# Performance work log

Measured on AMD Instinct MI355X. Metric: run time of the kernel, lower is better.

Reference implementation:

```python
import jax, jax.numpy as jnp
import numpy as np

P = 64        # patch size
NATOMS = 256  # dictionary atoms
N = 262144    # signal length
K = 262081    # npatches = N - P + 1 (stride-1 sliding patches)
M = 512       # measurement rows of A


def setup_inputs() -> dict:
    key = jax.random.key(0)
    k0, k1, k2, k3, k4, k5, k6 = jax.random.split(key, 7)
    d = jax.random.normal(k0, (1, P, NATOMS), jnp.float32) * 0.1
    x = jax.random.normal(k1, (NATOMS, K), jnp.float32) * 0.1
    ss = jnp.zeros((N, 1), jnp.float32)  # only its shape is used
    vb = (jax.random.uniform(k2, (N, 1)) > 0.05).astype(jnp.float32)
    # stride-1 sliding-window patch indices: column k covers [k, k+P)
    patches = (jnp.arange(K, dtype=jnp.int32)[None, :]
               + jnp.arange(P, dtype=jnp.int32)[:, None])  # [P, K]
    # npp = number of patches covering each signal sample
    npp = jnp.zeros((N, 1), jnp.float32).at[patches.reshape(-1), 0].add(1.0)
    sRef = jax.random.normal(k3, (N, 1), jnp.float32)
    A = jax.random.normal(k4, (M, N), jnp.float32) * 0.01
    Tarr = jax.random.normal(k5, (M, 1), jnp.float32)
    meanY = jnp.float32(0.1)
    ds = jax.random.normal(k6, (N, 1), jnp.float32)
    lam2 = jnp.float32(0.5)
    return {"d": d, "x": x, "ss": ss, "vb": vb, "patches": patches,
            "npp": npp, "sRef": sRef, "A": A, "Tarr": Tarr,
            "meanY": meanY, "ds": ds, "lam2": lam2, "npatches": K}


def reference(d, x, ss, vb, patches, npp, sRef, A, Tarr, meanY, ds, lam2, npatches):
    # ss_b[p, k] = (D @ X)[p, k] + meanY  -> per-patch reconstructions
    ss_b = jnp.squeeze(d) @ x + meanY                      # [P, K]
    # vectorized scatter-add replacing the torch loop over npatches
    ss_p_sum = jnp.zeros_like(ss).at[patches.reshape(-1), 0].add(ss_b.reshape(-1))  # [N,1]
    ss_f = (lam2 * ds + ss_p_sum) / (lam2 + npp)           # [N,1]
    ss_masked = ss_f * vb                                  # [N,1]
    Tref = A @ (ss_masked + sRef)                          # [M,1]
    return jnp.mean((Tref - Tarr) ** 2)
```

## Files before the change

### kernel.cpp

```cpp
#include <hip/hip_runtime.h>


namespace {
constexpr int kP = 64;
constexpr int kA = 256;
constexpr int kN = 262144;
constexpr int kK = 262081;
constexpr int kM = 512;

constexpr int CB = 256;
constexpr int OPT = 16;
constexpr int NB = CB * OPT;
constexpr int NCHUNK = kN / NB;
constexpr int NSPLIT = 8;
constexpr int APS = kA / NSPLIT;
constexpr int XS_LOG = NB + 64;
constexpr int XS_L4 = XS_LOG / 4;
constexpr int XS_P4 = 1304;
constexpr int R4 = XS_L4 + 1;
constexpr int GV_CH = 8;

__device__ __forceinline__ float f4c(const float4& v, int i) {
  switch (i & 3) {
    case 0: return v.x;
    case 1: return v.y;
    case 2: return v.z;
    default: return v.w;
  }
}

__device__ __forceinline__ void stage_row(const float* __restrict__ x,
                                          float* __restrict__ xsf,
                                          int a, int n0) {
  const int SA = (a + 1) & 3;
  const int gf = a * kK + n0 - 63 - SA;
  const int g4base = gf >> 2;
  const float4* __restrict__ x4 = (const float4*)x;
  const int g4max = (kA * kK) / 4 - 1;
  for (int r = threadIdx.x; r < R4; r += CB) {
    int g4 = g4base + r;
    g4 = g4 < 0 ? 0 : (g4 > g4max ? g4max : g4);
    float4 val = x4[g4];
#pragma unroll
    for (int w = 0; w < 4; ++w) {
      int i = 4 * r + w - SA;
      if ((unsigned)i < (unsigned)XS_LOG) {
        int k = n0 - 63 + i;
        float f = ((unsigned)k < (unsigned)kK) ? f4c(val, w) : 0.0f;
        xsf[i + 4 * (i >> 4)] = f;
      }
    }
  }
}

__device__ __forceinline__ void compute_atom(const float4* __restrict__ xs4,
                                             const float4* __restrict__ dt4,
                                             int a_loc, float* __restrict__ acc) {
  const int t4 = threadIdx.x * 4;
  float4 w[5];
#pragma unroll
  for (int q = 0; q < 4; ++q) {
    int l4 = t4 + q;
    w[q] = xs4[l4 + (l4 >> 2)];
  }
#pragma unroll
  for (int c = 0; c < 16; ++c) {
    {
      int l4 = t4 + c + 4;
      w[(c + 4) % 5] = xs4[l4 + (l4 >> 2)];
    }
    float4 D = dt4[a_loc * 16 + 15 - c];
    float dc[4] = {D.w, D.z, D.y, D.x};
#pragma unroll
    for (int i = 0; i < 4; ++i) {
      float coef = dc[i];
#pragma unroll
      for (int j = 0; j < OPT; ++j) {
        int off = i + j;
        float xv = f4c(w[(c + (off >> 2)) % 5], off & 3);
        acc[j] = fmaf(coef, xv, acc[j]);
      }
    }
  }
}

__global__ __launch_bounds__(CB, 2) void conv_kernel(const float* __restrict__ d,
                                                     const float* __restrict__ x,
                                                     float* __restrict__ sum) {
  __shared__ float4 xsA[XS_P4];
  __shared__ float4 xsB[XS_P4];
  __shared__ float4 dt4[APS * 16];
  const int n0 = blockIdx.x * NB;
  const int a0 = blockIdx.y * APS;
  const int tid = threadIdx.x;

  float* dtf = (float*)dt4;
#pragma unroll 1
  for (int i = tid; i < APS * kP; i += CB) {
    int al = i & (APS - 1);
    int p = i >> 5;
    dtf[al * kP + p] = d[p * kA + a0 + al];
  }

  float acc[OPT];
#pragma unroll
  for (int j = 0; j < OPT; ++j) acc[j] = 0.0f;

  stage_row(x, (float*)xsA, a0, n0);
  __syncthreads();

#pragma unroll 1
  for (int a = 0; a < APS; a += 2) {
    stage_row(x, (float*)xsB, a0 + a + 1, n0);
    compute_atom(xsA, dt4, a, acc);
    __syncthreads();
    if (a + 2 < APS) stage_row(x, (float*)xsA, a0 + a + 2, n0);
    compute_atom(xsB, dt4, a + 1, acc);
    __syncthreads();
  }

  const int nb = n0 + tid * OPT;
#pragma unroll
  for (int j = 0; j < OPT; ++j) atomicAdd(sum + nb + j, acc[j]);
}

__global__ void zero_kernel(float* __restrict__ sum, float* __restrict__ Tref) {
  const int i = blockIdx.x * blockDim.x + threadIdx.x;
  ((float4*)sum)[i] = make_float4(0.f, 0.f, 0.f, 0.f);
  if (i < kM / 4) ((float4*)Tref)[i] = make_float4(0.f, 0.f, 0.f, 0.f);
}

__global__ void vmask_kernel(const float* __restrict__ sum, const float* __restrict__ ds,
                             const float* __restrict__ npp, const float* __restrict__ vb,
                             const float* __restrict__ sRef,
                             const float* __restrict__ pMeanY,
                             const float* __restrict__ pLam2, float* __restrict__ v) {
  const int i = blockIdx.x * blockDim.x + threadIdx.x;
  const float meanY = pMeanY[0];
  const float lam2 = pLam2[0];
  const float4 s = ((const float4*)sum)[i];
  const float4 dd = ((const float4*)ds)[i];
  const float4 np = ((const float4*)npp)[i];
  const float4 vbv = ((const float4*)vb)[i];
  const float4 sr = ((const float4*)sRef)[i];
  float4 r;
  r.x = (lam2 * dd.x + s.x + meanY * np.x) / (lam2 + np.x) * vbv.x + sr.x;
  r.y = (lam2 * dd.y + s.y + meanY * np.y) / (lam2 + np.y) * vbv.y + sr.y;
  r.z = (lam2 * dd.z + s.z + meanY * np.z) / (lam2 + np.z) * vbv.z + sr.z;
  r.w = (lam2 * dd.w + s.w + meanY * np.w) / (lam2 + np.w) * vbv.w + sr.w;
  ((float4*)v)[i] = r;
}

__global__ __launch_bounds__(256) void gemv_kernel(const float* __restrict__ A,
                                                   const float* __restrict__ v,
                                                   float* __restrict__ Tref) {
  const int m = blockIdx.x >> 3;
  const int ch = blockIdx.x & (GV_CH - 1);
  const float4* __restrict__ A4 = (const float4*)(A + (size_t)m * kN);
  const float4* __restrict__ v4 = (const float4*)v;
  const int b0 = ch * (kN / 4 / GV_CH) + threadIdx.x;
  float s = 0.0f;
#pragma unroll 8
  for (int r = 0; r < 32; ++r) {
    float4 av = A4[b0 + r * 256];
    float4 vv = v4[b0 + r * 256];
    s = fmaf(av.x, vv.x, s);
    s = fmaf(av.y, vv.y, s);
    s = fmaf(av.z, vv.z, s);
    s = fmaf(av.w, vv.w, s);
  }
#pragma unroll
  for (int o = 32; o > 0; o >>= 1) s += __shfl_down(s, o, 64);
  if ((threadIdx.x & 63) == 0) atomicAdd(Tref + m, s);
}

__global__ void loss_kernel(const float* __restrict__ Tref, const float* __restrict__ Tarr,
                            float* __restrict__ out) {
  const int tid = threadIdx.x;
  float s = 0.0f;
  for (int i = tid; i < kM; i += 256) {
    float df = Tref[i] - Tarr[i];
    s = fmaf(df, df, s);
  }
#pragma unroll
  for (int o = 32; o > 0; o >>= 1) s += __shfl_down(s, o, 64);
  __shared__ float red[4];
  if ((tid & 63) == 0) red[tid >> 6] = s;
  __syncthreads();
  if (tid == 0) out[0] = (red[0] + red[1] + red[2] + red[3]) * (1.0f / kM);
}

}

extern "C" void kernel_launch(void* const* d_in, const int* in_sizes, int n_in,
                              void* d_out, int out_size, void* d_ws, size_t ws_size,
                              hipStream_t stream) {
  const float* d    = (const float*)d_in[0];
  const float* x    = (const float*)d_in[1];
  const float* vb   = (const float*)d_in[3];
  const float* npp  = (const float*)d_in[5];
  const float* sRef = (const float*)d_in[6];
  const float* A    = (const float*)d_in[7];
  const float* Tarr = (const float*)d_in[8];
  const float* pMeanY = (const float*)d_in[9];
  const float* ds   = (const float*)d_in[10];
  const float* pLam2 = (const float*)d_in[11];
  float* out = (float*)d_out;

  float* sum  = (float*)d_ws;
  float* v    = sum + kN;
  float* Tref = v + kN;

  zero_kernel<<<kN / 4 / 256, 256, 0, stream>>>(sum, Tref);
  conv_kernel<<<dim3(NCHUNK, NSPLIT), CB, 0, stream>>>(d, x, sum);
  vmask_kernel<<<kN / 4 / 256, 256, 0, stream>>>(sum, ds, npp, vb, sRef, pMeanY, pLam2, v);
  gemv_kernel<<<kM * GV_CH, 256, 0, stream>>>(A, v, Tref);
  loss_kernel<<<1, 256, 0, stream>>>(Tref, Tarr, out);
}
```

Baseline: 1.084 ms.

## Replace atomics with per-split partial buffers, double atom splits, batch staging loads

```diff
diff --git a/kernel.cpp b/kernel.cpp
--- a/kernel.cpp
+++ b/kernel.cpp
@@ -12,7 +12,7 @@
 constexpr int OPT = 16;
 constexpr int NB = CB * OPT;
 constexpr int NCHUNK = kN / NB;
-constexpr int NSPLIT = 8;
+constexpr int NSPLIT = 16;
 constexpr int APS = kA / NSPLIT;
 constexpr int XS_LOG = NB + 64;
 constexpr int XS_L4 = XS_LOG / 4;
@@ -20,6 +20,8 @@
 constexpr int R4 = XS_L4 + 1;
 constexpr int GV_CH = 8;
 
+static_assert(APS == 16, "transpose loop assumes APS==16");
+
 __device__ __forceinline__ float f4c(const float4& v, int i) {
   switch (i & 3) {
     case 0: return v.x;
@@ -31,23 +33,42 @@
 
 __device__ __forceinline__ void stage_row(const float* __restrict__ x,
                                           float* __restrict__ xsf,
-                                          int a, int n0) {
+                                          int a, int n0, int rlo, int rhi) {
   const int SA = (a + 1) & 3;
   const int gf = a * kK + n0 - 63 - SA;
   const int g4base = gf >> 2;
   const float4* __restrict__ x4 = (const float4*)x;
   const int g4max = (kA * kK) / 4 - 1;
-  for (int r = threadIdx.x; r < R4; r += CB) {
-    int g4 = g4base + r;
-    g4 = g4 < 0 ? 0 : (g4 > g4max ? g4max : g4);
-    float4 val = x4[g4];
-#pragma unroll
-    for (int w = 0; w < 4; ++w) {
-      int i = 4 * r + w - SA;
-      if ((unsigned)i < (unsigned)XS_LOG) {
-        int k = n0 - 63 + i;
-        float f = ((unsigned)k < (unsigned)kK) ? f4c(val, w) : 0.0f;
-        xsf[i + 4 * (i >> 4)] = f;
+  float4 vals[5];
+#pragma unroll
+  for (int u = 0; u < 5; ++u) {
+    int r = (int)threadIdx.x + u * CB;
+    if (r < R4) {
+      int g4 = g4base + r;
+      g4 = g4 < 0 ? 0 : (g4 > g4max ? g4max : g4);
+      vals[u] = x4[g4];
+    }
+  }
+#pragma unroll
+  for (int u = 0; u < 5; ++u) {
+    int r = (int)threadIdx.x + u * CB;
+    if (r >= R4) continue;
+    if (r >= rlo && r < rhi) {
+      const int i0 = 4 * r - SA;
+#pragma unroll
+      for (int w = 0; w < 4; ++w) {
+        int i = i0 + w;
+        xsf[i + 4 * (i >> 4)] = f4c(vals[u], w);
+      }
+    } else {
+#pragma unroll
+      for (int w = 0; w < 4; ++w) {
+        int i = 4 * r + w - SA;
+        if ((unsigned)i < (unsigned)XS_LOG) {
+          int k = n0 - 63 + i;
+          float f = ((unsigned)k < (unsigned)kK) ? f4c(vals[u], w) : 0.0f;
+          xsf[i + 4 * (i >> 4)] = f;
+        }
       }
     }
   }
@@ -84,21 +105,23 @@
   }
 }
 
-__global__ __launch_bounds__(CB, 2) void conv_kernel(const float* __restrict__ d,
+__global__ __launch_bounds__(CB, 3) void conv_kernel(const float* __restrict__ d,
                                                      const float* __restrict__ x,
-                                                     float* __restrict__ sum) {
+                                                     float* __restrict__ part) {
   __shared__ float4 xsA[XS_P4];
   __shared__ float4 xsB[XS_P4];
   __shared__ float4 dt4[APS * 16];
   const int n0 = blockIdx.x * NB;
   const int a0 = blockIdx.y * APS;
   const int tid = threadIdx.x;
+  const int rlo = (blockIdx.x == 0) ? 17 : 1;
+  const int rhi = (blockIdx.x == NCHUNK - 1) ? 1024 : 1040;
 
   float* dtf = (float*)dt4;
 #pragma unroll 1
   for (int i = tid; i < APS * kP; i += CB) {
     int al = i & (APS - 1);
-    int p = i >> 5;
+    int p = i >> 4;
     dtf[al * kP + p] = d[p * kA + a0 + al];
   }
 
@@ -106,31 +129,26 @@
 #pragma unroll
   for (int j = 0; j < OPT; ++j) acc[j] = 0.0f;
 
-  stage_row(x, (float*)xsA, a0, n0);
+  stage_row(x, (float*)xsA, a0, n0, rlo, rhi);
   __syncthreads();
 
 #pragma unroll 1
   for (int a = 0; a < APS; a += 2) {
-    stage_row(x, (float*)xsB, a0 + a + 1, n0);
+    stage_row(x, (float*)xsB, a0 + a + 1, n0, rlo, rhi);
     compute_atom(xsA, dt4, a, acc);
     __syncthreads();
-    if (a + 2 < APS) stage_row(x, (float*)xsA, a0 + a + 2, n0);
+    if (a + 2 < APS) stage_row(x, (float*)xsA, a0 + a + 2, n0, rlo, rhi);
     compute_atom(xsB, dt4, a + 1, acc);
     __syncthreads();
   }
 
-  const int nb = n0 + tid * OPT;
-#pragma unroll
-  for (int j = 0; j < OPT; ++j) atomicAdd(sum + nb + j, acc[j]);
-}
-
-__global__ void zero_kernel(float* __restrict__ sum, float* __restrict__ Tref) {
-  const int i = blockIdx.x * blockDim.x + threadIdx.x;
-  ((float4*)sum)[i] = make_float4(0.f, 0.f, 0.f, 0.f);
-  if (i < kM / 4) ((float4*)Tref)[i] = make_float4(0.f, 0.f, 0.f, 0.f);
-}
-
-__global__ void vmask_kernel(const float* __restrict__ sum, const float* __restrict__ ds,
+  float4* outp = (float4*)(part + (size_t)blockIdx.y * kN + n0 + tid * OPT);
+#pragma unroll
+  for (int j = 0; j < 4; ++j)
+    outp[j] = make_float4(acc[4 * j], acc[4 * j + 1], acc[4 * j + 2], acc[4 * j + 3]);
+}
+
+__global__ void vmask_kernel(const float* __restrict__ part, const float* __restrict__ ds,
                              const float* __restrict__ npp, const float* __restrict__ vb,
                              const float* __restrict__ sRef,
                              const float* __restrict__ pMeanY,
@@ -138,7 +156,12 @@
   const int i = blockIdx.x * blockDim.x + threadIdx.x;
   const float meanY = pMeanY[0];
   const float lam2 = pLam2[0];
-  const float4 s = ((const float4*)sum)[i];
+  float4 s = make_float4(0.f, 0.f, 0.f, 0.f);
+#pragma unroll
+  for (int c = 0; c < NSPLIT; ++c) {
+    float4 p = ((const float4*)(part + (size_t)c * kN))[i];
+    s.x += p.x; s.y += p.y; s.z += p.z; s.w += p.w;
+  }
   const float4 dd = ((const float4*)ds)[i];
   const float4 np = ((const float4*)npp)[i];
   const float4 vbv = ((const float4*)vb)[i];
@@ -153,7 +176,7 @@
 
 __global__ __launch_bounds__(256) void gemv_kernel(const float* __restrict__ A,
                                                    const float* __restrict__ v,
-                                                   float* __restrict__ Tref) {
+                                                   float* __restrict__ Tp) {
   const int m = blockIdx.x >> 3;
   const int ch = blockIdx.x & (GV_CH - 1);
   const float4* __restrict__ A4 = (const float4*)(A + (size_t)m * kN);
@@ -171,15 +194,21 @@
   }
 #pragma unroll
   for (int o = 32; o > 0; o >>= 1) s += __shfl_down(s, o, 64);
-  if ((threadIdx.x & 63) == 0) atomicAdd(Tref + m, s);
-}
-
-__global__ void loss_kernel(const float* __restrict__ Tref, const float* __restrict__ Tarr,
+  __shared__ float red[4];
+  if ((threadIdx.x & 63) == 0) red[threadIdx.x >> 6] = s;
+  __syncthreads();
+  if (threadIdx.x == 0) Tp[blockIdx.x] = red[0] + red[1] + red[2] + red[3];
+}
+
+__global__ void loss_kernel(const float* __restrict__ Tp, const float* __restrict__ Tarr,
                             float* __restrict__ out) {
   const int tid = threadIdx.x;
   float s = 0.0f;
-  for (int i = tid; i < kM; i += 256) {
-    float df = Tref[i] - Tarr[i];
+  for (int m = tid; m < kM; m += 256) {
+    float t = 0.0f;
+#pragma unroll
+    for (int c = 0; c < GV_CH; ++c) t += Tp[m * GV_CH + c];
+    float df = t - Tarr[m];
     s = fmaf(df, df, s);
   }
 #pragma unroll
@@ -207,13 +236,12 @@
   const float* pLam2 = (const float*)d_in[11];
   float* out = (float*)d_out;
 
-  float* sum  = (float*)d_ws;
-  float* v    = sum + kN;
-  float* Tref = v + kN;
-
-  zero_kernel<<<kN / 4 / 256, 256, 0, stream>>>(sum, Tref);
-  conv_kernel<<<dim3(NCHUNK, NSPLIT), CB, 0, stream>>>(d, x, sum);
-  vmask_kernel<<<kN / 4 / 256, 256, 0, stream>>>(sum, ds, npp, vb, sRef, pMeanY, pLam2, v);
-  gemv_kernel<<<kM * GV_CH, 256, 0, stream>>>(A, v, Tref);
-  loss_kernel<<<1, 256, 0, stream>>>(Tref, Tarr, out);
-}
+  float* part = (float*)d_ws;
+  float* v    = part + (size_t)NSPLIT * kN;
+  float* Tp   = v + kN;
+
+  conv_kernel<<<dim3(NCHUNK, NSPLIT), CB, 0, stream>>>(d, x, part);
+  vmask_kernel<<<kN / 4 / 256, 256, 0, stream>>>(part, ds, npp, vb, sRef, pMeanY, pLam2, v);
+  gemv_kernel<<<kM * GV_CH, 256, 0, stream>>>(A, v, Tp);
+  loss_kernel<<<1, 256, 0, stream>>>(Tp, Tarr, out);
+}
```

After: 1.130 ms. 1.04x slower.
